# Kernel optimization log

Measured on AMD Instinct MI355X. Metric: run time of the kernel, lower is better.

Reference implementation:

```python
import jax, jax.numpy as jnp
import numpy as np

B, S, H = 1, 2048, 4096
NH, NKV = 32, 8          # query heads, kv heads (GQA group = 4)
HD, VHD = 128, 128       # qk head_dim, v head_dim
ROPE = 64                # partial rotary dim (head_dim * 0.5)
NEG = -1e9


def setup_inputs() -> dict:
    key = jax.random.key(0)
    ks = jax.random.split(key, 6)
    hidden_states = jax.random.normal(ks[0], (B, S, H), dtype=jnp.float32)
    # real rotary embeddings, shape [1,1,S,ROPE] so they broadcast over heads
    inv_freq = 1.0 / (10000.0 ** (jnp.arange(0, ROPE, 2, dtype=jnp.float32) / ROPE))
    freqs = jnp.arange(S, dtype=jnp.float32)[:, None] * inv_freq[None, :]  # [S, ROPE/2]
    emb = jnp.concatenate([freqs, freqs], axis=-1)                          # [S, ROPE]
    cos = jnp.cos(emb)[None, None]  # [1,1,S,ROPE]
    sin = jnp.sin(emb)[None, None]
    # additive causal mask [1,1,S,S]
    causal = jnp.tril(jnp.ones((S, S), dtype=bool))
    attention_mask = jnp.where(causal, 0.0, NEG)[None, None].astype(jnp.float32)
    w_scale = 0.02
    Wq = jax.random.normal(ks[1], (H, NH * HD), dtype=jnp.float32) * w_scale
    Wk = jax.random.normal(ks[2], (H, NKV * HD), dtype=jnp.float32) * w_scale
    Wv = jax.random.normal(ks[3], (H, NKV * VHD), dtype=jnp.float32) * w_scale
    Wo = jax.random.normal(ks[4], (NH * VHD, H), dtype=jnp.float32) * w_scale
    sinks = jax.random.normal(ks[5], (NH,), dtype=jnp.float32)
    return {"hidden_states": hidden_states, "cos": cos, "sin": sin,
            "attention_mask": attention_mask, "Wq": Wq, "Wk": Wk, "Wv": Wv,
            "Wo": Wo, "sinks": sinks}


def _rotate_half(x):
    h = x.shape[-1] // 2
    return jnp.concatenate([-x[..., h:], x[..., :h]], axis=-1)


def reference(hidden_states, cos, sin, attention_mask, Wq, Wk, Wv, Wo, sinks):
    b, s, _ = hidden_states.shape
    scaling = HD ** -0.5
    # projections -> [b, heads, s, d]
    q = (hidden_states @ Wq).reshape(b, s, NH, HD).transpose(0, 2, 1, 3)
    k = (hidden_states @ Wk).reshape(b, s, NKV, HD).transpose(0, 2, 1, 3)
    v = (hidden_states @ Wv).reshape(b, s, NKV, VHD).transpose(0, 2, 1, 3)
    # partial RoPE on the first ROPE dims
    q_r, q_n = q[..., :ROPE], q[..., ROPE:]
    k_r, k_n = k[..., :ROPE], k[..., ROPE:]
    q_r = q_r * cos + _rotate_half(q_r) * sin
    k_r = k_r * cos + _rotate_half(k_r) * sin
    q = jnp.concatenate([q_r, q_n], axis=-1)
    k = jnp.concatenate([k_r, k_n], axis=-1)
    # GQA: repeat kv heads (repeat_interleave along head dim)
    n_rep = NH // NKV
    k = jnp.repeat(k, n_rep, axis=1)  # [b, NH, s, HD]
    v = jnp.repeat(v, n_rep, axis=1)  # [b, NH, s, VHD]
    scores = jnp.einsum('bhqd,bhkd->bhqk', q, k) * scaling + attention_mask
    # attention sinks: extra logit column per head, dropped after softmax
    sink_col = jnp.broadcast_to(sinks.reshape(1, NH, 1, 1), (b, NH, s, 1))
    logits = jnp.concatenate([scores, sink_col], axis=-1)
    w = jax.nn.softmax(logits.astype(jnp.float32), axis=-1).astype(q.dtype)[..., :-1]
    attn = jnp.einsum('bhqk,bhkd->bhqd', w, v)          # [b, NH, s, VHD]
    attn = attn.transpose(0, 2, 1, 3).reshape(b, s, NH * VHD)
    return attn @ Wo
```

## Files before the change

kernel.cpp:

```cpp
#include <hip/hip_runtime.h>
#include <hip/hip_bf16.h>
#include <cstdint>
#include <cstddef>

#define S_LEN 2048
#define NHEADS 32
#define NKVH   8
#define HDIM   128

using bf16x8 = __attribute__((ext_vector_type(8))) short;
using f32x4  = __attribute__((ext_vector_type(4))) float;
using f32x16 = __attribute__((ext_vector_type(16))) float;

__device__ __forceinline__ short f2bf(float f) {
  union { float f; unsigned u; } a; a.f = f;
  unsigned u = a.u;
  unsigned r = u + 0x7fffu + ((u >> 16) & 1u);
  return (short)(r >> 16);
}
__device__ __forceinline__ unsigned pack_bf2(float lo, float hi) {
  union { float f; unsigned u; } a, b; a.f = lo; b.f = hi;
  return __builtin_amdgcn_perm(b.u, a.u, 0x07060302);
}

__device__ __forceinline__ void gld16(const void* g, void* l) {
  __builtin_amdgcn_global_load_lds((__attribute__((address_space(1))) void*)(void*)g,
                                   (__attribute__((address_space(3))) void*)l, 16, 0, 0);
}

__global__ void cvt_f32_bf16(const float* __restrict__ x, short* __restrict__ y, int n4) {
  int i = blockIdx.x * blockDim.x + threadIdx.x;
  if (i >= n4) return;
  float4 v = reinterpret_cast<const float4*>(x)[i];
  short4 o;
  o.x = f2bf(v.x); o.y = f2bf(v.y); o.z = f2bf(v.z); o.w = f2bf(v.w);
  reinterpret_cast<short4*>(y)[i] = o;
}

__global__ __launch_bounds__(256)
void transpose_to_bf16(const float* __restrict__ W, short* __restrict__ Wt,
                       int K, int N) {
  __shared__ float tile[32 * 33];
  const int bn = blockIdx.x * 32, bk = blockIdx.y * 32;
  const int t = threadIdx.x;
  const int c4 = t & 7, kr = t >> 3;
  float4 v = *(const float4*)&W[(size_t)(bk + kr) * N + bn + c4 * 4];
  tile[kr * 33 + c4 * 4 + 0] = v.x;
  tile[kr * 33 + c4 * 4 + 1] = v.y;
  tile[kr * 33 + c4 * 4 + 2] = v.z;
  tile[kr * 33 + c4 * 4 + 3] = v.w;
  __syncthreads();
  const int k4 = t & 7, nr = t >> 3;
  short4 o;
  o.x = f2bf(tile[(k4 * 4 + 0) * 33 + nr]);
  o.y = f2bf(tile[(k4 * 4 + 1) * 33 + nr]);
  o.z = f2bf(tile[(k4 * 4 + 2) * 33 + nr]);
  o.w = f2bf(tile[(k4 * 4 + 3) * 33 + nr]);
  *(short4*)&Wt[(size_t)(bn + nr) * K + bk + k4 * 4] = o;
}

__global__ __launch_bounds__(256)
void gemm_qkv(const short* __restrict__ A, const short* __restrict__ B,
              short* __restrict__ Qb, short* __restrict__ Kb, short* __restrict__ Vtb,
              const float* __restrict__ cosb, const float* __restrict__ sinb) {
  const int K = 4096;
  __shared__ short smem[16896];
  const int bn = blockIdx.x * 128;
  const int bm = blockIdx.y * 128;
  const int t = threadIdx.x;
  const int lane = t & 63;
  const int wave = t >> 6;
  const int wm = (wave >> 1) * 64;
  const int wn = (wave & 1) * 64;
  const int lr = lane & 15;
  const int lk = (lane >> 4) * 8;

  f32x4 acc[4][4] = {};

  const int arow = t >> 2;
  const int acol = (t & 3) * 8;
  const size_t ab0 = (size_t)(bm + arow) * K + acol;
  const size_t ab1 = (size_t)(bm + 64 + arow) * K + acol;
  const size_t bb0 = (size_t)(bn + arow) * K + acol;
  const size_t bb1 = (size_t)(bn + 64 + arow) * K + acol;

  auto stage = [&](int k0, int b) {
    char* base = (char*)smem + b * 16384 + t * 16;
    gld16(A + ab0 + k0, base);
    gld16(A + ab1 + k0, base + 4096);
    gld16(B + bb0 + k0, base + 8192);
    gld16(B + bb1 + k0, base + 12288);
  };

  stage(0, 0);
  for (int it = 0; it < 128; ++it) {
    __syncthreads();
    if (it + 1 < 128) stage((it + 1) * 32, (it + 1) & 1);
    const short* Asb = smem + (it & 1) * 8192;
    const short* Bsb = Asb + 4096;
    bf16x8 af[4], bfr[4];
#pragma unroll
    for (int i = 0; i < 4; ++i)
      af[i] = *(const bf16x8*)&Asb[(wm + i * 16 + lr) * 32 + lk];
#pragma unroll
    for (int j = 0; j < 4; ++j)
      bfr[j] = *(const bf16x8*)&Bsb[(wn + j * 16 + lr) * 32 + lk];
#pragma unroll
    for (int i = 0; i < 4; ++i)
#pragma unroll
      for (int j = 0; j < 4; ++j)
        acc[i][j] = __builtin_amdgcn_mfma_f32_16x16x32_bf16(af[i], bfr[j], acc[i][j], 0, 0, 0);
  }

  const int cr = (lane >> 4) << 2;
  const int cc = lane & 15;
  const int region = (bn >= 5120) ? 2 : (bn >= 4096 ? 1 : 0);

  if (region < 2) {
    if (wn == 0) {
#pragma unroll
      for (int i = 0; i < 4; ++i) {
#pragma unroll
        for (int r = 0; r < 4; ++r) {
          int srow = bm + wm + i * 16 + cr + r;
#pragma unroll
          for (int j = 0; j < 2; ++j) {
            int c = j * 16 + cc;
            float cv = cosb[srow * 64 + c];
            float sv = sinb[srow * 64 + c];
            float x1 = acc[i][j][r], x2 = acc[i][j + 2][r];
            acc[i][j][r]     = x1 * cv - x2 * sv;
            acc[i][j + 2][r] = x2 * cv + x1 * sv;
          }
        }
      }
    }
#pragma unroll
    for (int i = 0; i < 4; ++i)
#pragma unroll
      for (int j = 0; j < 4; ++j) {
        int row = bm + wm + i * 16 + cr;
        int col = bn + wn + j * 16 + cc;
#pragma unroll
        for (int r = 0; r < 4; ++r) {
          short v = f2bf(acc[i][j][r]);
          if (region == 0) Qb[(size_t)(row + r) * 4096 + col] = v;
          else             Kb[(size_t)(row + r) * 1024 + (col - 4096)] = v;
        }
      }
  } else {
    __syncthreads();
#pragma unroll
    for (int i = 0; i < 4; ++i)
#pragma unroll
      for (int j = 0; j < 4; ++j) {
        int lc = wn + j * 16 + cc;
        int lrow = wm + i * 16 + cr;
#pragma unroll
        for (int r = 0; r < 4; ++r)
          smem[lc * 132 + lrow + r] = f2bf(acc[i][j][r]);
      }
    __syncthreads();
    const int rowl = t >> 1;
    const int off = (t & 1) * 64;
    short* dst = Vtb + (size_t)(bn - 5120 + rowl) * 2048 + bm + off;
#pragma unroll
    for (int c = 0; c < 8; ++c)
      *(bf16x8*)(dst + c * 8) = *(const bf16x8*)&smem[rowl * 132 + off + c * 8];
  }
}

__global__ __launch_bounds__(256, 2)
void gemm_out(const short* __restrict__ A, const short* __restrict__ B,
              float* __restrict__ C) {
  const int K = 4096, N = 4096;
  __shared__ short smem[32768];
  const int bn = blockIdx.x * 128;
  const int bm = blockIdx.y * 128;
  const int t = threadIdx.x;
  const int lane = t & 63;
  const int wave = t >> 6;
  const int wm = (wave >> 1) * 64;
  const int wn = (wave & 1) * 64;
  const int lr = lane & 15;
  const int lk3 = lane >> 4;

  f32x4 acc[4][4] = {};

  const int srow = t >> 3;
  const int sch = (t & 7) ^ ((srow & 1) << 2);
  const size_t ab = (size_t)(bm + srow) * K + sch * 8;
  const size_t bb = (size_t)(bn + srow) * K + sch * 8;

  auto stage = [&](int k0, int b) {
    short* dst = smem + b * 16384 + t * 8;
#pragma unroll
    for (int p = 0; p < 4; ++p) {
      gld16(A + ab + k0 + (size_t)(p * 32) * K, dst + p * 2048);
      gld16(B + bb + k0 + (size_t)(p * 32) * K, dst + 8192 + p * 2048);
    }
  };

  stage(0, 0);
  for (int it = 0; it < 64; ++it) {
    __syncthreads();
    if (it + 1 < 64) stage((it + 1) * 64, (it + 1) & 1);
    const short* Asb = smem + (it & 1) * 16384;
    const short* Bsb = Asb + 8192;
#pragma unroll
    for (int h = 0; h < 2; ++h) {
      bf16x8 af[4], bfr[4];
#pragma unroll
      for (int i = 0; i < 4; ++i) {
        int row = wm + i * 16 + lr;
        af[i] = *(const bf16x8*)&Asb[row * 64 + (((h * 4 + lk3) ^ ((row & 1) << 2)) * 8)];
      }
#pragma unroll
      for (int j = 0; j < 4; ++j) {
        int row = wn + j * 16 + lr;
        bfr[j] = *(const bf16x8*)&Bsb[row * 64 + (((h * 4 + lk3) ^ ((row & 1) << 2)) * 8)];
      }
#pragma unroll
      for (int i = 0; i < 4; ++i)
#pragma unroll
        for (int j = 0; j < 4; ++j)
          acc[i][j] = __builtin_amdgcn_mfma_f32_16x16x32_bf16(af[i], bfr[j], acc[i][j], 0, 0, 0);
    }
  }

  const int cr = (lane >> 4) << 2;
  const int cc = lane & 15;
#pragma unroll
  for (int i = 0; i < 4; ++i)
#pragma unroll
    for (int j = 0; j < 4; ++j) {
      int row = bm + wm + i * 16 + cr;
      int col = bn + wn + j * 16 + cc;
#pragma unroll
      for (int r = 0; r < 4; ++r)
        C[(size_t)(row + r) * N + col] = acc[i][j][r];
    }
}

__global__ __launch_bounds__(256, 2)
void attn_kernel(const short* __restrict__ Q, const short* __restrict__ Kg,
                 const short* __restrict__ Vg, const float* __restrict__ sinks,
                 short* __restrict__ O) {
  __shared__ short lds[32768];
  const int h = blockIdx.x;
  const int qt = 15 - blockIdx.y;
  const int q0 = qt * 128;
  const int kvh = h >> 2;
  const int t = threadIdx.x;
  const int lane = t & 63;
  const int w = t >> 6;
  const int l31 = lane & 31;
  const int l7 = lane & 7;
  const bool qh = lane >= 32;
  const int q5 = qh ? 1 : 0;
  const int nkt = 2 * qt + 2;

  const int kch = (t & 15) ^ ((t >> 4) & 7);
  const short* kgb = Kg + (size_t)(t >> 4) * 1024 + kvh * 128 + kch * 8;
  const int vch = (t & 7) ^ ((t >> 3) & 7);
  const short* vgb = Vg + (size_t)(kvh * 128 + (t >> 3)) * 2048 + vch * 8;

  auto stage = [&](int kt, int b) {
    short* kl = lds + b * 16384 + t * 8;
    short* vl = lds + b * 16384 + 8192 + t * 8;
    const short* kg = kgb + (size_t)kt * 64 * 1024;
    const short* vg = vgb + kt * 64;
#pragma unroll
    for (int c = 0; c < 4; ++c) {
      gld16(kg + (size_t)c * 16 * 1024, kl + c * 2048);
      gld16(vg + (size_t)c * 32 * 2048, vl + c * 2048);
    }
  };

  const short* qp = Q + (size_t)(q0 + w * 32 + l31) * 4096 + h * 128 + q5 * 8;
  bf16x8 qf[8];
#pragma unroll
  for (int st = 0; st < 8; ++st) qf[st] = *(const bf16x8*)(qp + st * 16);

  union { short s[8]; bf16x8 v; } ones;
#pragma unroll
  for (int i = 0; i < 8; ++i) ones.s[i] = (short)0x3F80;

  f32x16 acc[4] = {};
  f32x16 lacc = {};

  stage(0, 0);
  const int qg = q0 + w * 32 + l31;
  const float ce = 0.12751743f;

  for (int kt = 0; kt < nkt; ++kt) {
    const int b = kt & 1;
    __syncthreads();
    if (kt + 1 < nkt) stage(kt + 1, b ^ 1);
    const short* Ks = lds + b * 16384;
    const short* Vs = Ks + 8192;

    f32x16 sa0 = {}, sa1 = {};
#pragma unroll
    for (int st = 0; st < 8; ++st) {
      const int cp = ((st * 2 + q5) ^ l7) * 8;
      bf16x8 k0 = *(const bf16x8*)(Ks + (l31) * 128 + cp);
      bf16x8 k1 = *(const bf16x8*)(Ks + (32 + l31) * 128 + cp);
      sa0 = __builtin_amdgcn_mfma_f32_32x32x16_bf16(k0, qf[st], sa0, 0, 0, 0);
      sa1 = __builtin_amdgcn_mfma_f32_32x32x16_bf16(k1, qf[st], sa1, 0, 0, 0);
    }

    if (kt >= 2 * qt) {
      const int kb0 = kt * 64 + q5 * 4;
#pragma unroll
      for (int r = 0; r < 16; ++r) {
        int kg0 = kb0 + ((r >> 2) << 3) + (r & 3);
        float s0 = (kg0 <= qg) ? sa0[r] * ce : -INFINITY;
        float s1 = (kg0 + 32 <= qg) ? sa1[r] * ce : -INFINITY;
        sa0[r] = __builtin_amdgcn_exp2f(s0);
        sa1[r] = __builtin_amdgcn_exp2f(s1);
      }
    } else {
#pragma unroll
      for (int r = 0; r < 16; ++r) {
        sa0[r] = __builtin_amdgcn_exp2f(sa0[r] * ce);
        sa1[r] = __builtin_amdgcn_exp2f(sa1[r] * ce);
      }
    }

#pragma unroll
    for (int s = 0; s < 4; ++s) {
      const f32x16& S = (s & 2) ? sa1 : sa0;
      float a0, a1, a2, a3, b0, b1, b2, b3;
      if (s & 1) {
        a0 = qh ? S[12] : S[8];  a1 = qh ? S[13] : S[9];
        a2 = qh ? S[14] : S[10]; a3 = qh ? S[15] : S[11];
        b0 = qh ? S[8]  : S[12]; b1 = qh ? S[9]  : S[13];
        b2 = qh ? S[10] : S[14]; b3 = qh ? S[11] : S[15];
      } else {
        a0 = qh ? S[4] : S[0]; a1 = qh ? S[5] : S[1];
        a2 = qh ? S[6] : S[2]; a3 = qh ? S[7] : S[3];
        b0 = qh ? S[0] : S[4]; b1 = qh ? S[1] : S[5];
        b2 = qh ? S[2] : S[6]; b3 = qh ? S[3] : S[7];
      }
      unsigned d0 = pack_bf2(a0, a1), d1 = pack_bf2(a2, a3);
      unsigned e0 = pack_bf2(b0, b1), e1 = pack_bf2(b2, b3);
      unsigned r0 = (unsigned)__shfl_xor((int)e0, 32, 64);
      unsigned r1 = (unsigned)__shfl_xor((int)e1, 32, 64);
      union { unsigned u[4]; bf16x8 v; } P;
      P.u[0] = qh ? r0 : d0;  P.u[1] = qh ? r1 : d1;
      P.u[2] = qh ? d0 : r0;  P.u[3] = qh ? d1 : r1;

      lacc = __builtin_amdgcn_mfma_f32_32x32x16_bf16(ones.v, P.v, lacc, 0, 0, 0);
#pragma unroll
      for (int m = 0; m < 4; ++m) {
        bf16x8 vf = *(const bf16x8*)(Vs + (m * 32 + l31) * 64 + (((s * 2 + q5) ^ l7) * 8));
        acc[m] = __builtin_amdgcn_mfma_f32_32x32x16_bf16(vf, P.v, acc[m], 0, 0, 0);
      }
    }
  }

  float denom = lacc[0] + __builtin_amdgcn_exp2f(sinks[h] * 1.4426950f);
  float rinv = 1.0f / denom;

  __syncthreads();
#pragma unroll
  for (int m = 0; m < 4; ++m) {
#pragma unroll
    for (int r = 0; r < 16; ++r) {
      int d = m * 32 + ((r >> 2) << 3) + q5 * 4 + (r & 3);
      int ql = w * 32 + l31;
      lds[ql * 128 + (((d >> 3) ^ l7) << 3) + (d & 7)] = f2bf(acc[m][r] * rinv);
    }
  }
  __syncthreads();
  const int qrow = t >> 1;
  const int half = (t & 1) * 8;
  short* ob = O + (size_t)(q0 + qrow) * 4096 + h * 128;
#pragma unroll
  for (int cc = 0; cc < 8; ++cc) {
    int chunk = half + cc;
    bf16x8 v = *(const bf16x8*)&lds[qrow * 128 + ((chunk ^ (qrow & 7)) << 3)];
    *(bf16x8*)(ob + chunk * 8) = v;
  }
}

extern "C" void kernel_launch(void* const* d_in, const int* in_sizes, int n_in,
                              void* d_out, int out_size, void* d_ws, size_t ws_size,
                              hipStream_t stream) {
  const float* hs    = (const float*)d_in[0];
  const float* cosb  = (const float*)d_in[1];
  const float* sinb  = (const float*)d_in[2];
  const float* Wq    = (const float*)d_in[4];
  const float* Wk    = (const float*)d_in[5];
  const float* Wv    = (const float*)d_in[6];
  const float* Wo    = (const float*)d_in[7];
  const float* sinks = (const float*)d_in[8];
  float* out = (float*)d_out;

  char* ws = (char*)d_ws;
  short* Xb    = (short*)ws;
  short* Wqkvt = (short*)(ws + 16777216);
  short* Qb    = (short*)(ws + 67108864);
  short* Kb    = (short*)(ws + 83886080);
  short* Vtb   = (short*)(ws + 88080384);
  short* Ab    = Xb;
  short* Wot   = Wqkvt;

  cvt_f32_bf16<<<8192, 256, 0, stream>>>(hs, Xb, 2097152);
  transpose_to_bf16<<<dim3(128, 128), 256, 0, stream>>>(Wq, Wqkvt, 4096, 4096);
  transpose_to_bf16<<<dim3(32, 128), 256, 0, stream>>>(Wk, Wqkvt + (size_t)4096 * 4096, 4096, 1024);
  transpose_to_bf16<<<dim3(32, 128), 256, 0, stream>>>(Wv, Wqkvt + (size_t)5120 * 4096, 4096, 1024);

  gemm_qkv<<<dim3(48, 16), 256, 0, stream>>>(Xb, Wqkvt, Qb, Kb, Vtb, cosb, sinb);

  transpose_to_bf16<<<dim3(128, 128), 256, 0, stream>>>(Wo, Wot, 4096, 4096);

  attn_kernel<<<dim3(32, 16), 256, 0, stream>>>(Qb, Kb, Vtb, sinks, Ab);

  gemm_out<<<dim3(32, 16), 256, 0, stream>>>(Ab, Wot, out);
}
```

Before: 486.4 us.

## Enlarge QKV GEMM tile to 256x256 with deeper software pipelined LDS staging

The QKV projection GEMM now uses 256x256 output tiles computed by 512 threads (8 waves, each owning a 128x64 sub-tile). It uses 128KB of dynamic shared memory to keep two 64-wide K tiles in flight. Loads are staged in half-tiles and synchronized with explicit vmcnt waits and raw barriers, and s_setprio is raised around the MFMA bursts so global loads overlap with math. The goal is higher operand reuse and fewer LDS and global reads per FLOP. In exchange the grid shrinks to 192 blocks, fewer than the CU count, and the large LDS footprint limits occupancy to one block per CU. The V-transpose epilogue is done in two halves to fit the LDS staging buffer.

```diff
diff --git a/kernel.cpp b/kernel.cpp
--- a/kernel.cpp
+++ b/kernel.cpp
@@ -27,6 +27,10 @@
   __builtin_amdgcn_global_load_lds((__attribute__((address_space(1))) void*)(void*)g,
                                    (__attribute__((address_space(3))) void*)l, 16, 0, 0);
 }
+
+#define VMWAIT(N) asm volatile("s_waitcnt vmcnt(" #N ")" ::: "memory")
+#define SCHEDB()  __builtin_amdgcn_sched_barrier(0)
+#define MFMA16(a, b, c) __builtin_amdgcn_mfma_f32_16x16x32_bf16((a), (b), (c), 0, 0, 0)
 
 __global__ void cvt_f32_bf16(const float* __restrict__ x, short* __restrict__ y, int n4) {
   int i = blockIdx.x * blockDim.x + threadIdx.x;
@@ -59,67 +63,117 @@
   *(short4*)&Wt[(size_t)(bn + nr) * K + bk + k4 * 4] = o;
 }
 
-__global__ __launch_bounds__(256)
+#define QKV_TILE(TT, VM1, VM3, S12, S34) {                                         \
+    const short* Ar = smem + ((TT) & 1) * 16384;                                   \
+    const short* Br = smem + 32768 + ((TT) & 1) * 16384;                           \
+    VMWAIT(VM1);                                                                   \
+    __builtin_amdgcn_s_barrier();                                                  \
+    SCHEDB();                                                                      \
+    bf16x8 af[8], b0, b1;                                                          \
+    _Pragma("unroll") for (int i = 0; i < 8; ++i)                                  \
+      af[i] = *(const bf16x8*)&Ar[(wm + i * 16 + lr) * 32 + l4 * 8];               \
+    b0 = *(const bf16x8*)&Br[(wn +  0 + lr) * 32 + l4 * 8];                        \
+    b1 = *(const bf16x8*)&Br[(wn + 16 + lr) * 32 + l4 * 8];                        \
+    if (S12) stageA((TT) + 1, 1);                                                  \
+    __builtin_amdgcn_s_setprio(1);                                                 \
+    _Pragma("unroll") for (int i = 0; i < 8; ++i) {                                \
+      acc[i][0] = MFMA16(af[i], b0, acc[i][0]);                                    \
+      acc[i][1] = MFMA16(af[i], b1, acc[i][1]);                                    \
+    }                                                                              \
+    __builtin_amdgcn_s_setprio(0);                                                 \
+    b0 = *(const bf16x8*)&Br[(wn + 32 + lr) * 32 + l4 * 8];                        \
+    b1 = *(const bf16x8*)&Br[(wn + 48 + lr) * 32 + l4 * 8];                        \
+    if (S12) stageB((TT) + 1, 1);                                                  \
+    __builtin_amdgcn_s_setprio(1);                                                 \
+    _Pragma("unroll") for (int i = 0; i < 8; ++i) {                                \
+      acc[i][2] = MFMA16(af[i], b0, acc[i][2]);                                    \
+      acc[i][3] = MFMA16(af[i], b1, acc[i][3]);                                    \
+    }                                                                              \
+    __builtin_amdgcn_s_setprio(0);                                                 \
+    VMWAIT(VM3);                                                                   \
+    __builtin_amdgcn_s_barrier();                                                  \
+    SCHEDB();                                                                      \
+    const short* Ar1 = Ar + 8192;                                                  \
+    const short* Br1 = Br + 8192;                                                  \
+    _Pragma("unroll") for (int i = 0; i < 8; ++i)                                  \
+      af[i] = *(const bf16x8*)&Ar1[(wm + i * 16 + lr) * 32 + l4 * 8];              \
+    b0 = *(const bf16x8*)&Br1[(wn +  0 + lr) * 32 + l4 * 8];                       \
+    b1 = *(const bf16x8*)&Br1[(wn + 16 + lr) * 32 + l4 * 8];                       \
+    if (S34) stageA((TT) + 2, 0);                                                  \
+    __builtin_amdgcn_s_setprio(1);                                                 \
+    _Pragma("unroll") for (int i = 0; i < 8; ++i) {                                \
+      acc[i][0] = MFMA16(af[i], b0, acc[i][0]);                                    \
+      acc[i][1] = MFMA16(af[i], b1, acc[i][1]);                                    \
+    }                                                                              \
+    __builtin_amdgcn_s_setprio(0);                                                 \
+    b0 = *(const bf16x8*)&Br1[(wn + 32 + lr) * 32 + l4 * 8];                       \
+    b1 = *(const bf16x8*)&Br1[(wn + 48 + lr) * 32 + l4 * 8];                       \
+    if (S34) stageB((TT) + 2, 0);                                                  \
+    __builtin_amdgcn_s_setprio(1);                                                 \
+    _Pragma("unroll") for (int i = 0; i < 8; ++i) {                                \
+      acc[i][2] = MFMA16(af[i], b0, acc[i][2]);                                    \
+      acc[i][3] = MFMA16(af[i], b1, acc[i][3]);                                    \
+    }                                                                              \
+    __builtin_amdgcn_s_setprio(0);                                                 \
+  }
+
+__global__ __launch_bounds__(512, 2)
 void gemm_qkv(const short* __restrict__ A, const short* __restrict__ B,
               short* __restrict__ Qb, short* __restrict__ Kb, short* __restrict__ Vtb,
               const float* __restrict__ cosb, const float* __restrict__ sinb) {
   const int K = 4096;
-  __shared__ short smem[16896];
-  const int bn = blockIdx.x * 128;
-  const int bm = blockIdx.y * 128;
+  extern __shared__ __align__(16) short smem[];
+  const int bn = blockIdx.x * 256;
+  const int bm = blockIdx.y * 256;
   const int t = threadIdx.x;
   const int lane = t & 63;
-  const int wave = t >> 6;
-  const int wm = (wave >> 1) * 64;
-  const int wn = (wave & 1) * 64;
+  const int w = t >> 6;
+  const int wm = (w >> 2) * 128;
+  const int wn = (w & 3) * 64;
   const int lr = lane & 15;
-  const int lk = (lane >> 4) * 8;
-
-  f32x4 acc[4][4] = {};
-
-  const int arow = t >> 2;
-  const int acol = (t & 3) * 8;
-  const size_t ab0 = (size_t)(bm + arow) * K + acol;
-  const size_t ab1 = (size_t)(bm + 64 + arow) * K + acol;
-  const size_t bb0 = (size_t)(bn + arow) * K + acol;
-  const size_t bb1 = (size_t)(bn + 64 + arow) * K + acol;
-
-  auto stage = [&](int k0, int b) {
-    char* base = (char*)smem + b * 16384 + t * 16;
-    gld16(A + ab0 + k0, base);
-    gld16(A + ab1 + k0, base + 4096);
-    gld16(B + bb0 + k0, base + 8192);
-    gld16(B + bb1 + k0, base + 12288);
+  const int l4 = lane >> 4;
+
+  f32x4 acc[8][4] = {};
+
+  const int srow0 = w * 16 + (lane >> 2);
+  const int srow1 = (8 + w) * 16 + (lane >> 2);
+  const int sch   = (lane & 3) * 8;
+  const size_t ga0 = (size_t)(bm + srow0) * K + sch;
+  const size_t ga1 = (size_t)(bm + srow1) * K + sch;
+  const size_t gb0 = (size_t)(bn + srow0) * K + sch;
+  const size_t gb1 = (size_t)(bn + srow1) * K + sch;
+  const int ldl0 = w * 512 + lane * 8;
+  const int ldl1 = (8 + w) * 512 + lane * 8;
+
+  auto stageA = [&](int kt, int kh) {
+    const int ko = kt * 64 + kh * 32;
+    short* rb = smem + (kt & 1) * 16384 + kh * 8192;
+    gld16(A + ga0 + ko, rb + ldl0);
+    gld16(A + ga1 + ko, rb + ldl1);
   };
-
-  stage(0, 0);
-  for (int it = 0; it < 128; ++it) {
-    __syncthreads();
-    if (it + 1 < 128) stage((it + 1) * 32, (it + 1) & 1);
-    const short* Asb = smem + (it & 1) * 8192;
-    const short* Bsb = Asb + 4096;
-    bf16x8 af[4], bfr[4];
-#pragma unroll
-    for (int i = 0; i < 4; ++i)
-      af[i] = *(const bf16x8*)&Asb[(wm + i * 16 + lr) * 32 + lk];
-#pragma unroll
-    for (int j = 0; j < 4; ++j)
-      bfr[j] = *(const bf16x8*)&Bsb[(wn + j * 16 + lr) * 32 + lk];
-#pragma unroll
-    for (int i = 0; i < 4; ++i)
-#pragma unroll
-      for (int j = 0; j < 4; ++j)
-        acc[i][j] = __builtin_amdgcn_mfma_f32_16x16x32_bf16(af[i], bfr[j], acc[i][j], 0, 0, 0);
-  }
+  auto stageB = [&](int kt, int kh) {
+    const int ko = kt * 64 + kh * 32;
+    short* rb = smem + 32768 + (kt & 1) * 16384 + kh * 8192;
+    gld16(B + gb0 + ko, rb + ldl0);
+    gld16(B + gb1 + ko, rb + ldl1);
+  };
+
+  stageA(0, 0); stageB(0, 0);
+  stageA(0, 1); stageB(0, 1);
+  stageA(1, 0); stageB(1, 0);
+
+  for (int kt = 0; kt < 62; ++kt) QKV_TILE(kt, 8, 8, 1, 1);
+  QKV_TILE(62, 8, 8, 1, 0);
+  QKV_TILE(63, 4, 0, 0, 0);
 
   const int cr = (lane >> 4) << 2;
   const int cc = lane & 15;
   const int region = (bn >= 5120) ? 2 : (bn >= 4096 ? 1 : 0);
 
   if (region < 2) {
-    if (wn == 0) {
-#pragma unroll
-      for (int i = 0; i < 4; ++i) {
+    if ((wn & 64) == 0) {
+#pragma unroll
+      for (int i = 0; i < 8; ++i) {
 #pragma unroll
         for (int r = 0; r < 4; ++r) {
           int srow = bm + wm + i * 16 + cr + r;
@@ -136,7 +190,7 @@
       }
     }
 #pragma unroll
-    for (int i = 0; i < 4; ++i)
+    for (int i = 0; i < 8; ++i)
 #pragma unroll
       for (int j = 0; j < 4; ++j) {
         int row = bm + wm + i * 16 + cr;
@@ -151,22 +205,28 @@
   } else {
     __syncthreads();
 #pragma unroll
-    for (int i = 0; i < 4; ++i)
-#pragma unroll
-      for (int j = 0; j < 4; ++j) {
-        int lc = wn + j * 16 + cc;
-        int lrow = wm + i * 16 + cr;
-#pragma unroll
-        for (int r = 0; r < 4; ++r)
-          smem[lc * 132 + lrow + r] = f2bf(acc[i][j][r]);
-      }
-    __syncthreads();
-    const int rowl = t >> 1;
-    const int off = (t & 1) * 64;
-    short* dst = Vtb + (size_t)(bn - 5120 + rowl) * 2048 + bm + off;
-#pragma unroll
-    for (int c = 0; c < 8; ++c)
-      *(bf16x8*)(dst + c * 8) = *(const bf16x8*)&smem[rowl * 132 + off + c * 8];
+    for (int h = 0; h < 2; ++h) {
+      if ((wm >> 7) == h) {
+#pragma unroll
+        for (int i = 0; i < 8; ++i)
+#pragma unroll
+          for (int j = 0; j < 4; ++j) {
+            int lc = wn + j * 16 + cc;
+            int lrow = i * 16 + cr;
+#pragma unroll
+            for (int r = 0; r < 4; ++r)
+              smem[lc * 132 + lrow + r] = f2bf(acc[i][j][r]);
+          }
+      }
+      __syncthreads();
+      int colx = t >> 1;
+      int off = (t & 1) * 64;
+      short* dst = Vtb + (size_t)(bn - 5120 + colx) * 2048 + bm + h * 128 + off;
+#pragma unroll
+      for (int c8 = 0; c8 < 8; ++c8)
+        *(bf16x8*)(dst + c8 * 8) = *(const bf16x8*)&smem[colx * 132 + off + c8 * 8];
+      if (h == 0) __syncthreads();
+    }
   }
 }
 
@@ -398,6 +458,13 @@
   const float* sinks = (const float*)d_in[8];
   float* out = (float*)d_out;
 
+  static bool attr_done = false;
+  if (!attr_done) {
+    hipFuncSetAttribute(reinterpret_cast<const void*>(&gemm_qkv),
+                        hipFuncAttributeMaxDynamicSharedMemorySize, 131072);
+    attr_done = true;
+  }
+
   char* ws = (char*)d_ws;
   short* Xb    = (short*)ws;
   short* Wqkvt = (short*)(ws + 16777216);
@@ -412,7 +479,7 @@
   transpose_to_bf16<<<dim3(32, 128), 256, 0, stream>>>(Wk, Wqkvt + (size_t)4096 * 4096, 4096, 1024);
   transpose_to_bf16<<<dim3(32, 128), 256, 0, stream>>>(Wv, Wqkvt + (size_t)5120 * 4096, 4096, 1024);
 
-  gemm_qkv<<<dim3(48, 16), 256, 0, stream>>>(Xb, Wqkvt, Qb, Kb, Vtb, cosb, sinb);
+  gemm_qkv<<<dim3(24, 8), 512, 131072, stream>>>(Xb, Wqkvt, Qb, Kb, Vtb, cosb, sinb);
 
   transpose_to_bf16<<<dim3(128, 128), 256, 0, stream>>>(Wo, Wot, 4096, 4096);
 
```

New measurement: 475.1 us. 2.3% less time.
